# Performance work log

Hardware: AMD Instinct MI355X
Metric: run time of the kernel (lower is better)

Reference implementation:

```python
import jax, jax.numpy as jnp
import numpy as np

N, K, D = 524288, 32, 8
EPS = 1e-6


def setup_inputs() -> dict:
    key = jax.random.key(0)
    k1, k2, k3, k4 = jax.random.split(key, 4)
    x = jax.random.normal(k1, (N, D), dtype=jnp.float32)
    pi = jax.random.uniform(k2, (K,), dtype=jnp.float32)
    means = jax.random.normal(k3, (K, D), dtype=jnp.float32)
    # eye + small perturbation keeps tril(chol_var) well-conditioned (PD covariance)
    chol_var = jnp.eye(D, dtype=jnp.float32)[None] + 0.1 * jax.random.normal(k4, (K, D, D), dtype=jnp.float32)
    return {"x": x, "pi": pi, "means": means, "chol_var": chol_var}


def reference(x, pi, means, chol_var):
    d = x.shape[-1]
    L = jnp.tril(chol_var)                                   # [K,d,d]
    cov = jnp.einsum('kij,klj->kil', L, L) + EPS * jnp.eye(d, dtype=x.dtype)
    C = jnp.linalg.cholesky(cov)                             # [K,d,d] (MVN recomputes cholesky)
    logdet = 2.0 * jnp.sum(jnp.log(jnp.diagonal(C, axis1=-2, axis2=-1)), axis=-1)  # [K]
    eye = jnp.eye(d, dtype=x.dtype)
    Cinv = jax.vmap(lambda c: jax.scipy.linalg.solve_triangular(c, eye, lower=True))(C)  # [K,d,d]
    zx = jnp.einsum('kij,nj->nki', Cinv, x)                  # [N,K,d]
    zm = jnp.einsum('kij,kj->ki', Cinv, means)               # [K,d]
    maha = jnp.sum((zx - zm[None]) ** 2, axis=-1)            # [N,K]
    log_2pi = jnp.log(2.0 * jnp.pi).astype(x.dtype)
    log_probs = -0.5 * (maha + d * log_2pi + logdet[None])   # [N,K]
    wll = log_probs + jax.nn.log_softmax(pi)[None]
    return jax.scipy.special.logsumexp(wll, axis=1)          # [N]
```

## Files before the change

kernel.cpp:

```cpp
#include <hip/hip_runtime.h>
#include <math.h>

#define K_ 32
#define D_ 8
#define NF 48
#define NTHREADS 256
#define NBLOCKS 1024
#define TPW 4

typedef _Float16 half8 __attribute__((ext_vector_type(8)));
typedef float f32x16 __attribute__((ext_vector_type(16)));

__global__ __launch_bounds__(NTHREADS) void gmm_mfma(
    const float* __restrict__ x,
    const float* __restrict__ pi,
    const float* __restrict__ means,
    const float* __restrict__ chol,
    float* __restrict__ out)
{
    __shared__ __align__(16) _Float16 ldsA[3][64][8];

    const int tid  = threadIdx.x;
    const int lane = tid & 63;
    const int m    = lane & 31;
    const bool h1  = lane >= 32;

    const int w  = blockIdx.x * (NTHREADS / 64) + (tid >> 6);
    const int t0 = w * TPW;
    const float4* xp = (const float4*)x;

    float xv[TPW][D_];
    if (tid >= 64) {
#pragma unroll
        for (int u = 0; u < TPW; ++u) {
            const int n = (t0 + u) * 32 + m;
            float4 a = xp[2 * n], b2 = xp[2 * n + 1];
            xv[u][0] = a.x;  xv[u][1] = a.y;  xv[u][2] = a.z;  xv[u][3] = a.w;
            xv[u][4] = b2.x; xv[u][5] = b2.y; xv[u][6] = b2.z; xv[u][7] = b2.w;
        }
    }

    if (tid < K_) {
        const int k = tid;

        float M[D_][D_];
        {
            const float4* cp = (const float4*)(chol + k * 64);
#pragma unroll
            for (int i = 0; i < D_; ++i) {
                float4 a = cp[2 * i];
                M[i][0] = a.x; M[i][1] = a.y; M[i][2] = a.z; M[i][3] = a.w;
                if (i >= 4) {
                    float4 bq = cp[2 * i + 1];
                    M[i][4] = bq.x; M[i][5] = bq.y; M[i][6] = bq.z; M[i][7] = bq.w;
                }
            }
        }

        float rd[D_];
#pragma unroll
        for (int i = 0; i < D_; ++i) rd[i] = 1.f / M[i][i];

        float logdet = 0.f;
#pragma unroll
        for (int i = 0; i < D_; ++i) logdet += __logf(fabsf(rd[i]));
        logdet *= -2.f;

#pragma unroll
        for (int j = 0; j < D_; ++j) {
            M[j][j] = rd[j];
#pragma unroll
            for (int i = j + 1; i < D_; ++i) {
                float s = 0.f;
#pragma unroll
                for (int mm = j; mm < i; ++mm) s += M[i][mm] * M[mm][j];
                M[i][j] = -s * rd[i];
            }
        }

#pragma unroll
        for (int i = 0; i < D_; ++i) {
            float t[D_];
#pragma unroll
            for (int j = 0; j <= i; ++j) {
                float s = 0.f;
#pragma unroll
                for (int mm = i; mm < D_; ++mm) s += M[mm][i] * M[mm][j];
                t[j] = s;
            }
#pragma unroll
            for (int j = 0; j <= i; ++j) M[i][j] = t[j];
        }

        float b[D_], q = 0.f;
        {
            const float4* mp = (const float4*)(means + k * 8);
            float4 ma = mp[0], mb = mp[1];
            float mu[D_] = {ma.x, ma.y, ma.z, ma.w, mb.x, mb.y, mb.z, mb.w};
#pragma unroll
            for (int i = 0; i < D_; ++i) {
                float s = 0.f;
#pragma unroll
                for (int j = 0; j <= i; ++j) s += M[i][j] * mu[j];
#pragma unroll
                for (int j = i + 1; j < D_; ++j) s += M[j][i] * mu[j];
                b[i] = s;
                q += s * mu[i];
            }
        }

        float lse;
        {
            float mx = pi[0];
#pragma unroll
            for (int t = 1; t < K_; ++t) mx = fmaxf(mx, pi[t]);
            float se = 0.f;
#pragma unroll
            for (int t = 0; t < K_; ++t) se += __expf(pi[t] - mx);
            lse = mx + __logf(se);
        }

        const float LOG2PI = 1.8378770664093453f;
        const float LOG2E  = 1.4426950408889634f;
        const float ALPHA  = 0.72134752044448170f;
        float cst2 = ((pi[k] - lse) - 0.5f * (logdet + 8.f * LOG2PI)) * LOG2E;

        float V[NF];
        {
            int t = 0;
#pragma unroll
            for (int i = 0; i < D_; ++i)
#pragma unroll
                for (int j = 0; j <= i; ++j)
                    V[t++] = (i == j) ? -ALPHA * M[i][i] : -2.f * ALPHA * M[i][j];
#pragma unroll
            for (int i = 0; i < D_; ++i) V[36 + i] = 2.f * ALPHA * b[i];
            V[44] = cst2 - ALPHA * q;
            V[45] = 0.f; V[46] = 0.f; V[47] = 0.f;
        }

#pragma unroll
        for (int s = 0; s < 3; ++s)
#pragma unroll
            for (int h = 0; h < 2; ++h) {
                half8 hv;
#pragma unroll
                for (int j = 0; j < 8; ++j) hv[j] = (_Float16)V[16 * s + 8 * h + j];
                *(half8*)&ldsA[s][h * 32 + k][0] = hv;
            }
    }
    __syncthreads();

    if (tid < 64) {
#pragma unroll
        for (int u = 0; u < TPW; ++u) {
            const int n = (t0 + u) * 32 + m;
            float4 a = xp[2 * n], b2 = xp[2 * n + 1];
            xv[u][0] = a.x;  xv[u][1] = a.y;  xv[u][2] = a.z;  xv[u][3] = a.w;
            xv[u][4] = b2.x; xv[u][5] = b2.y; xv[u][6] = b2.z; xv[u][7] = b2.w;
        }
    }

    half8 wf[3];
#pragma unroll
    for (int s = 0; s < 3; ++s) wf[s] = *(const half8*)&ldsA[s][lane][0];

    const float LN2 = 0.69314718055994531f;

#pragma unroll
    for (int u = 0; u < TPW; ++u) {
        float Y[NF];
        {
            int t = 0;
#pragma unroll
            for (int i = 0; i < D_; ++i)
#pragma unroll
                for (int j = 0; j <= i; ++j) Y[t++] = xv[u][i] * xv[u][j];
#pragma unroll
            for (int i = 0; i < D_; ++i) Y[36 + i] = xv[u][i];
            Y[44] = 1.f; Y[45] = 0.f; Y[46] = 0.f; Y[47] = 0.f;
        }

        f32x16 acc;
#pragma unroll
        for (int r = 0; r < 16; ++r) acc[r] = 0.f;

#pragma unroll
        for (int s = 0; s < 3; ++s) {
            half8 bf;
#pragma unroll
            for (int j = 0; j < 8; ++j) {
                float v = h1 ? Y[16 * s + 8 + j] : Y[16 * s + j];
                bf[j] = (_Float16)v;
            }
            acc = __builtin_amdgcn_mfma_f32_32x32x16_f16(wf[s], bf, acc, 0, 0, 0);
        }

        float tot = 0.f;
#pragma unroll
        for (int r = 0; r < 16; ++r) tot += exp2f(acc[r]);
        tot += __shfl_xor(tot, 32, 64);
        float res = log2f(tot) * LN2;
        if (!h1) out[(t0 + u) * 32 + m] = res;
    }
}

extern "C" void kernel_launch(void* const* d_in, const int* in_sizes, int n_in,
                              void* d_out, int out_size, void* d_ws, size_t ws_size,
                              hipStream_t stream) {
    const float* x     = (const float*)d_in[0];
    const float* pi    = (const float*)d_in[1];
    const float* means = (const float*)d_in[2];
    const float* chol  = (const float*)d_in[3];
    float* out = (float*)d_out;
    (void)in_sizes; (void)n_in; (void)out_size; (void)d_ws; (void)ws_size;

    gmm_mfma<<<NBLOCKS, NTHREADS, 0, stream>>>(x, pi, means, chol, out);
}
```

Before: 75.73 us.

## Split per-component parameter prep into a separate single-block kernel

Moves the per-component Cholesky inversion, precision matrix, mean terms and log-softmax of pi out of every block into a one-block prep kernel that writes fp16 MFMA weight fragments to workspace. The main kernel then loads those fragments straight from global memory, with no LDS staging and no __syncthreads. This removes prep work repeated in all 1024 blocks and the block-wide stall while it runs. The cost is a second kernel launch and a serial dependency between the two launches.

```diff
diff --git a/kernel.cpp b/kernel.cpp
--- a/kernel.cpp
+++ b/kernel.cpp
@@ -11,15 +11,128 @@
 typedef _Float16 half8 __attribute__((ext_vector_type(8)));
 typedef float f32x16 __attribute__((ext_vector_type(16)));
 
-__global__ __launch_bounds__(NTHREADS) void gmm_mfma(
-    const float* __restrict__ x,
+
+__global__ void gmm_prep(
     const float* __restrict__ pi,
     const float* __restrict__ means,
     const float* __restrict__ chol,
+    _Float16* __restrict__ wsV)
+{
+    const int k = threadIdx.x;
+    if (k >= K_) return;
+
+    float M[D_][D_];
+    {
+        const float4* cp = (const float4*)(chol + k * 64);
+#pragma unroll
+        for (int i = 0; i < D_; ++i) {
+            float4 a = cp[2 * i];
+            M[i][0] = a.x; M[i][1] = a.y; M[i][2] = a.z; M[i][3] = a.w;
+            if (i >= 4) {
+                float4 bq = cp[2 * i + 1];
+                M[i][4] = bq.x; M[i][5] = bq.y; M[i][6] = bq.z; M[i][7] = bq.w;
+            }
+        }
+    }
+
+    float rd[D_];
+#pragma unroll
+    for (int i = 0; i < D_; ++i) rd[i] = 1.f / M[i][i];
+
+    float logdet = 0.f;
+#pragma unroll
+    for (int i = 0; i < D_; ++i) logdet += __logf(fabsf(rd[i]));
+    logdet *= -2.f;
+
+#pragma unroll
+    for (int j = 0; j < D_; ++j) {
+        M[j][j] = rd[j];
+#pragma unroll
+        for (int i = j + 1; i < D_; ++i) {
+            float s = 0.f;
+#pragma unroll
+            for (int mm = j; mm < i; ++mm) s += M[i][mm] * M[mm][j];
+            M[i][j] = -s * rd[i];
+        }
+    }
+
+#pragma unroll
+    for (int i = 0; i < D_; ++i) {
+        float t[D_];
+#pragma unroll
+        for (int j = 0; j <= i; ++j) {
+            float s = 0.f;
+#pragma unroll
+            for (int mm = i; mm < D_; ++mm) s += M[mm][i] * M[mm][j];
+            t[j] = s;
+        }
+#pragma unroll
+        for (int j = 0; j <= i; ++j) M[i][j] = t[j];
+    }
+
+    float b[D_], q = 0.f;
+    {
+        const float4* mp = (const float4*)(means + k * 8);
+        float4 ma = mp[0], mb = mp[1];
+        float mu[D_] = {ma.x, ma.y, ma.z, ma.w, mb.x, mb.y, mb.z, mb.w};
+#pragma unroll
+        for (int i = 0; i < D_; ++i) {
+            float s = 0.f;
+#pragma unroll
+            for (int j = 0; j <= i; ++j) s += M[i][j] * mu[j];
+#pragma unroll
+            for (int j = i + 1; j < D_; ++j) s += M[j][i] * mu[j];
+            b[i] = s;
+            q += s * mu[i];
+        }
+    }
+
+    float lse;
+    {
+        float mx = pi[0];
+#pragma unroll
+        for (int t = 1; t < K_; ++t) mx = fmaxf(mx, pi[t]);
+        float se = 0.f;
+#pragma unroll
+        for (int t = 0; t < K_; ++t) se += __expf(pi[t] - mx);
+        lse = mx + __logf(se);
+    }
+
+    const float LOG2PI = 1.8378770664093453f;
+    const float LOG2E  = 1.4426950408889634f;
+    const float ALPHA  = 0.72134752044448170f;
+    float cst2 = ((pi[k] - lse) - 0.5f * (logdet + 8.f * LOG2PI)) * LOG2E;
+
+    float V[NF];
+    {
+        int t = 0;
+#pragma unroll
+        for (int i = 0; i < D_; ++i)
+#pragma unroll
+            for (int j = 0; j <= i; ++j)
+                V[t++] = (i == j) ? -ALPHA * M[i][i] : -2.f * ALPHA * M[i][j];
+#pragma unroll
+        for (int i = 0; i < D_; ++i) V[36 + i] = 2.f * ALPHA * b[i];
+        V[44] = cst2 - ALPHA * q;
+        V[45] = 0.f; V[46] = 0.f; V[47] = 0.f;
+    }
+
+#pragma unroll
+    for (int s = 0; s < 3; ++s)
+#pragma unroll
+        for (int h = 0; h < 2; ++h) {
+            half8 hv;
+#pragma unroll
+            for (int j = 0; j < 8; ++j) hv[j] = (_Float16)V[16 * s + 8 * h + j];
+            *(half8*)&wsV[(s * 64 + h * 32 + k) * 8] = hv;
+        }
+}
+
+__global__ __launch_bounds__(NTHREADS) void gmm_mfma(
+    const float* __restrict__ x,
+    const _Float16* __restrict__ wsV,
     float* __restrict__ out)
 {
-    __shared__ __align__(16) _Float16 ldsA[3][64][8];
-
     const int tid  = threadIdx.x;
     const int lane = tid & 63;
     const int m    = lane & 31;
@@ -28,144 +141,21 @@
     const int w  = blockIdx.x * (NTHREADS / 64) + (tid >> 6);
     const int t0 = w * TPW;
     const float4* xp = (const float4*)x;
+    const float LN2 = 0.69314718055994531f;
 
     float xv[TPW][D_];
-    if (tid >= 64) {
-#pragma unroll
-        for (int u = 0; u < TPW; ++u) {
-            const int n = (t0 + u) * 32 + m;
-            float4 a = xp[2 * n], b2 = xp[2 * n + 1];
-            xv[u][0] = a.x;  xv[u][1] = a.y;  xv[u][2] = a.z;  xv[u][3] = a.w;
-            xv[u][4] = b2.x; xv[u][5] = b2.y; xv[u][6] = b2.z; xv[u][7] = b2.w;
-        }
-    }
-
-    if (tid < K_) {
-        const int k = tid;
-
-        float M[D_][D_];
-        {
-            const float4* cp = (const float4*)(chol + k * 64);
-#pragma unroll
-            for (int i = 0; i < D_; ++i) {
-                float4 a = cp[2 * i];
-                M[i][0] = a.x; M[i][1] = a.y; M[i][2] = a.z; M[i][3] = a.w;
-                if (i >= 4) {
-                    float4 bq = cp[2 * i + 1];
-                    M[i][4] = bq.x; M[i][5] = bq.y; M[i][6] = bq.z; M[i][7] = bq.w;
-                }
-            }
-        }
-
-        float rd[D_];
-#pragma unroll
-        for (int i = 0; i < D_; ++i) rd[i] = 1.f / M[i][i];
-
-        float logdet = 0.f;
-#pragma unroll
-        for (int i = 0; i < D_; ++i) logdet += __logf(fabsf(rd[i]));
-        logdet *= -2.f;
-
-#pragma unroll
-        for (int j = 0; j < D_; ++j) {
-            M[j][j] = rd[j];
-#pragma unroll
-            for (int i = j + 1; i < D_; ++i) {
-                float s = 0.f;
-#pragma unroll
-                for (int mm = j; mm < i; ++mm) s += M[i][mm] * M[mm][j];
-                M[i][j] = -s * rd[i];
-            }
-        }
-
-#pragma unroll
-        for (int i = 0; i < D_; ++i) {
-            float t[D_];
-#pragma unroll
-            for (int j = 0; j <= i; ++j) {
-                float s = 0.f;
-#pragma unroll
-                for (int mm = i; mm < D_; ++mm) s += M[mm][i] * M[mm][j];
-                t[j] = s;
-            }
-#pragma unroll
-            for (int j = 0; j <= i; ++j) M[i][j] = t[j];
-        }
-
-        float b[D_], q = 0.f;
-        {
-            const float4* mp = (const float4*)(means + k * 8);
-            float4 ma = mp[0], mb = mp[1];
-            float mu[D_] = {ma.x, ma.y, ma.z, ma.w, mb.x, mb.y, mb.z, mb.w};
-#pragma unroll
-            for (int i = 0; i < D_; ++i) {
-                float s = 0.f;
-#pragma unroll
-                for (int j = 0; j <= i; ++j) s += M[i][j] * mu[j];
-#pragma unroll
-                for (int j = i + 1; j < D_; ++j) s += M[j][i] * mu[j];
-                b[i] = s;
-                q += s * mu[i];
-            }
-        }
-
-        float lse;
-        {
-            float mx = pi[0];
-#pragma unroll
-            for (int t = 1; t < K_; ++t) mx = fmaxf(mx, pi[t]);
-            float se = 0.f;
-#pragma unroll
-            for (int t = 0; t < K_; ++t) se += __expf(pi[t] - mx);
-            lse = mx + __logf(se);
-        }
-
-        const float LOG2PI = 1.8378770664093453f;
-        const float LOG2E  = 1.4426950408889634f;
-        const float ALPHA  = 0.72134752044448170f;
-        float cst2 = ((pi[k] - lse) - 0.5f * (logdet + 8.f * LOG2PI)) * LOG2E;
-
-        float V[NF];
-        {
-            int t = 0;
-#pragma unroll
-            for (int i = 0; i < D_; ++i)
-#pragma unroll
-                for (int j = 0; j <= i; ++j)
-                    V[t++] = (i == j) ? -ALPHA * M[i][i] : -2.f * ALPHA * M[i][j];
-#pragma unroll
-            for (int i = 0; i < D_; ++i) V[36 + i] = 2.f * ALPHA * b[i];
-            V[44] = cst2 - ALPHA * q;
-            V[45] = 0.f; V[46] = 0.f; V[47] = 0.f;
-        }
-
-#pragma unroll
-        for (int s = 0; s < 3; ++s)
-#pragma unroll
-            for (int h = 0; h < 2; ++h) {
-                half8 hv;
-#pragma unroll
-                for (int j = 0; j < 8; ++j) hv[j] = (_Float16)V[16 * s + 8 * h + j];
-                *(half8*)&ldsA[s][h * 32 + k][0] = hv;
-            }
-    }
-    __syncthreads();
-
-    if (tid < 64) {
-#pragma unroll
-        for (int u = 0; u < TPW; ++u) {
-            const int n = (t0 + u) * 32 + m;
-            float4 a = xp[2 * n], b2 = xp[2 * n + 1];
-            xv[u][0] = a.x;  xv[u][1] = a.y;  xv[u][2] = a.z;  xv[u][3] = a.w;
-            xv[u][4] = b2.x; xv[u][5] = b2.y; xv[u][6] = b2.z; xv[u][7] = b2.w;
-        }
-    }
-
+#pragma unroll
+    for (int u = 0; u < TPW; ++u) {
+        const int n = (t0 + u) * 32 + m;
+        float4 a = xp[2 * n], b2 = xp[2 * n + 1];
+        xv[u][0] = a.x;  xv[u][1] = a.y;  xv[u][2] = a.z;  xv[u][3] = a.w;
+        xv[u][4] = b2.x; xv[u][5] = b2.y; xv[u][6] = b2.z; xv[u][7] = b2.w;
+    }
+
+    const half8* wp = (const half8*)wsV;
     half8 wf[3];
 #pragma unroll
-    for (int s = 0; s < 3; ++s) wf[s] = *(const half8*)&ldsA[s][lane][0];
-
-    const float LN2 = 0.69314718055994531f;
+    for (int s = 0; s < 3; ++s) wf[s] = wp[s * 64 + lane];
 
 #pragma unroll
     for (int u = 0; u < TPW; ++u) {
@@ -213,7 +203,9 @@
     const float* means = (const float*)d_in[2];
     const float* chol  = (const float*)d_in[3];
     float* out = (float*)d_out;
-    (void)in_sizes; (void)n_in; (void)out_size; (void)d_ws; (void)ws_size;
-
-    gmm_mfma<<<NBLOCKS, NTHREADS, 0, stream>>>(x, pi, means, chol, out);
+    _Float16* wsV = (_Float16*)d_ws;
+    (void)in_sizes; (void)n_in; (void)out_size; (void)ws_size;
+
+    gmm_prep<<<1, 64, 0, stream>>>(pi, means, chol, wsV);
+    gmm_mfma<<<NBLOCKS, NTHREADS, 0, stream>>>(x, wsV, out);
 }
```

Result: no change. 74.79 us (-1.2%).
